# Optimization experiments

Hardware: AMD Instinct MI355X
Metric: run time of the kernel (lower is better)

The kernel has to match this reference:

```python
import jax, jax.numpy as jnp
import numpy as np
import math

B, T, Z, H, DOF = 256, 200, 64, 256, 12
NUM_LINKS = 13
POS_DIM = (NUM_LINKS + 1) * 3  # 42
TIME_BANDS = 6
TIME_DIM = 2 * TIME_BANDS + 1  # 13
ACTION_SCALE = 0.25
TRACK_ALPHA = 1.0
SIGMA_MIN, SIGMA_MAX = 0.05, 0.5


def setup_inputs() -> dict:
    key = jax.random.key(0)
    ks = iter(jax.random.split(key, 32))
    rn = lambda shape, s=0.1: jax.random.normal(next(ks), shape, jnp.float32) * s
    inp = {
        'z': jax.random.normal(next(ks), (B, Z), jnp.float32),
        'W_hz': rn((H, Z)), 'b_hz': rn((H,)),
        'W_cz': rn((H, Z)), 'b_cz': rn((H,)),
        'Wih': rn((4 * H, DOF + Z + TIME_DIM)), 'Whh': rn((4 * H, H)),
        'bih': rn((4 * H,)), 'bhh': rn((4 * H,)),
        'Wp1': rn((H, H)), 'bp1': rn((H,)),
        'Wp2': rn((DOF, H)), 'bp2': rn((DOF,)),
        'Wo1': rn((H, H)), 'bo1': rn((H,)),
        'Wo2': rn((3, H)), 'bo2': rn((3,)),
        'Wv': rn((POS_DIM, H)), 'bv': rn((POS_DIM,)),
        'Wfk': rn((NUM_LINKS * 3, DOF)), 'bfk': rn((NUM_LINKS * 3,)),
        'pos_mean': jax.random.normal(next(ks), (NUM_LINKS + 1, 3), jnp.float32),
        'pos_std': 0.5 + jax.random.uniform(next(ks), (NUM_LINKS + 1, 3), jnp.float32),
        'joint_lower': -jnp.ones((DOF,), jnp.float32),
        'joint_upper': jnp.ones((DOF,), jnp.float32),
        'default_dof_pos': jnp.zeros((DOF,), jnp.float32),
    }
    return inp


def _time_features():
    t = jnp.linspace(0.0, 1.0, T)
    feats = [t]
    for k in range(TIME_BANDS):
        f = 2.0 ** k
        feats.append(jnp.sin(2 * math.pi * f * t))
        feats.append(jnp.cos(2 * math.pi * f * t))
    return jnp.stack(feats, axis=-1)  # [T, TIME_DIM]


def reference(z, W_hz, b_hz, W_cz, b_cz, Wih, Whh, bih, bhh,
              Wp1, bp1, Wp2, bp2, Wo1, bo1, Wo2, bo2, Wv, bv, Wfk, bfk,
              pos_mean, pos_std, joint_lower, joint_upper, default_dof_pos):
    joint_range = (joint_upper - joint_lower) / 2.0
    joint_mean = (joint_upper + joint_lower) / 2.0
    time_feats = _time_features()  # [T, TIME_DIM]

    h0 = z @ W_hz.T + b_hz  # [B,H]
    c0 = z @ W_cz.T + b_cz
    prev0 = jnp.broadcast_to(default_dof_pos, (B, DOF))

    def step(carry, tf):
        h, c, prev = carry
        prev_norm = (prev - joint_mean) / joint_range
        x = jnp.concatenate([prev_norm, z, jnp.broadcast_to(tf, (B, TIME_DIM))], axis=-1)
        g = x @ Wih.T + bih + h @ Whh.T + bhh  # [B,4H]
        i, f, gg, o = jnp.split(g, 4, axis=-1)
        c_new = jax.nn.sigmoid(f) * c + jax.nn.sigmoid(i) * jnp.tanh(gg)
        h_new = jax.nn.sigmoid(o) * jnp.tanh(c_new)
        action = jnp.tanh(jax.nn.relu(h_new @ Wp1.T + bp1) @ Wp2.T + bp2)
        target = action * ACTION_SCALE + default_dof_pos
        cur = prev + TRACK_ALPHA * (target - prev)
        clamped = jnp.clip(cur, joint_lower, joint_upper)
        cur_in = cur + jax.lax.stop_gradient(clamped - cur)  # straight-through clamp
        obj = jax.nn.relu(h_new @ Wo1.T + bo1) @ Wo2.T + bo2
        return (h_new, c_new, jax.lax.stop_gradient(cur_in)), (h_new, action, cur, obj)

    _, (H_seq, actions, joints, objs) = jax.lax.scan(step, (h0, c0, prev0), time_feats)
    # [T,B,*] -> [B,T,*]
    H_seq = jnp.swapaxes(H_seq, 0, 1)
    actions_seq = jnp.swapaxes(actions, 0, 1)
    joint_traj = jnp.swapaxes(joints, 0, 1)
    object_traj = jnp.swapaxes(objs, 0, 1)

    agent_traj = joint_traj @ Wfk.T + bfk  # FK: [B,T,39]
    combined = jnp.concatenate([agent_traj, object_traj], axis=-1)  # [B,T,42]
    combined_rs = combined.reshape(B, T, NUM_LINKS + 1, 3)
    graph_x_mu = ((combined_rs - pos_mean) / pos_std).reshape(B, T, POS_DIM)

    sigma = SIGMA_MIN + (SIGMA_MAX - SIGMA_MIN) * jax.nn.sigmoid(H_seq @ Wv.T + bv)
    log_sigma_pos = jnp.log(sigma)
    return (graph_x_mu, joint_traj, actions_seq, log_sigma_pos)
```

## Files before the change

kernel.cpp:

```cpp
#include <hip/hip_runtime.h>
#include <math.h>

#define B_ 256
#define T_ 200
#define H_ 256
#define DOF_ 12

typedef __bf16 bf16;
typedef __bf16 bf16x8 __attribute__((ext_vector_type(8)));
typedef float f32x4 __attribute__((ext_vector_type(4)));

#define XK 288
#define XPAD 296
#define P1PAD 264

#define PI_D 3.14159265358979323846

#define OFF_TF     0u
#define OFF_TCONP  10400u
#define OFF_ZCP    829600u
#define OFF_H0     1878176u
#define OFF_C0     2140320u
#define OFF_WCOMB  2402464u
#define OFF_WP1    2992288u
#define OFF_WP2    3123360u
#define OFF_WO1    3131552u
#define OFF_WO2    3262624u
#define OFF_WV     3270816u
#define OFF_HX     3295392u
#define OFF_FLAGS  3557536u
#define OFF_HSEQ   3558400u

__device__ __forceinline__ float sigf(float x) { return 1.f / (1.f + __expf(-x)); }
__device__ __forceinline__ float tanh_f(float x) {
  float a = fabsf(x);
  float e = __expf(-2.f * a);
  float t = (1.f - e) / (1.f + e);
  return x < 0.f ? -t : t;
}

#define LBAR() asm volatile("s_waitcnt lgkmcnt(0)\n\ts_barrier" ::: "memory")

__global__ void k_zflags(unsigned int* flags) {
  int i = threadIdx.x;
  if (i < 32)
    __hip_atomic_store(&flags[i], 0u, __ATOMIC_RELAXED, __HIP_MEMORY_SCOPE_AGENT);
}

__global__ void k_tfeat(float* tf) {
  int i = blockIdx.x * blockDim.x + threadIdx.x;
  if (i >= T_ * 13) return;
  int t = i / 13, j = i % 13;
  float tv = (float)t / 199.f;
  float v;
  if (j == 0) v = tv;
  else {
    int k = (j - 1) >> 1;
    float f = (float)(1 << k);
    double arg = 2.0 * PI_D * (double)f * (double)tv;
    v = (j & 1) ? (float)sin(arg) : (float)cos(arg);
  }
  tf[i] = v;
}

__global__ void k_prep(const float* __restrict__ tf, const float* __restrict__ Wih,
                       const float* __restrict__ z,
                       const float* __restrict__ bih, const float* __restrict__ bhh,
                       const float* __restrict__ Whz, const float* __restrict__ bhz,
                       const float* __restrict__ Wcz, const float* __restrict__ bcz,
                       float* tconp, float* zcp, float* h0, float* c0) {
  int i = blockIdx.x * blockDim.x + threadIdx.x;
  if (i < 204800) {
    int g = i & 3, q = i >> 2;
    int m = q & 127, hm = (q >> 7) & 1, t = q >> 8;
    int n = g * 256 + 128 * hm + m;
    float s = 0.f;
    #pragma unroll
    for (int j = 0; j < 13; ++j) s += tf[t * 13 + j] * Wih[n * 89 + 76 + j];
    tconp[i] = s;
    return;
  }
  i -= 204800;
  if (i < 262144) {
    int r = i & 3, g = (i >> 2) & 3, tid = (i >> 4) & 511;
    int half = (i >> 13) & 1, pairk = i >> 14;
    int wv = tid >> 6, lr = tid & 15, lq = (tid >> 4) & 3;
    int b = pairk * 16 + lq * 4 + r;
    int n = g * 256 + 128 * half + 16 * wv + lr;
    float s = bih[n] + bhh[n];
    for (int k = 0; k < 64; ++k) s += z[b * 64 + k] * Wih[n * 89 + 12 + k];
    zcp[i] = s;
    return;
  }
  i -= 262144;
  if (i < 65536) {
    int b = i / 256, u = i % 256;
    float s = bhz[u];
    for (int k = 0; k < 64; ++k) s += z[b * 64 + k] * Whz[u * 64 + k];
    h0[i] = s;
    return;
  }
  i -= 65536;
  if (i < 65536) {
    int b = i / 256, u = i % 256;
    float s = bcz[u];
    for (int k = 0; k < 64; ++k) s += z[b * 64 + k] * Wcz[u * 64 + k];
    c0[i] = s;
  }
}

__global__ void k_cast(const float* __restrict__ Whh, const float* __restrict__ Wih,
                       const float* __restrict__ Wp1, const float* __restrict__ Wp2,
                       const float* __restrict__ Wo1, const float* __restrict__ Wo2,
                       const float* __restrict__ Wv,
                       bf16* Wcomb, bf16* Wp1b, bf16* Wp2b, bf16* Wo1b,
                       bf16* Wo2b, bf16* Wvb) {
  int i = blockIdx.x * blockDim.x + threadIdx.x;
  if (i < 294912) {
    int n = i / XK, k = i % XK;
    float v = (k < 256) ? Whh[n * 256 + k]
            : ((k < 268) ? Wih[n * 89 + (k - 256)] : 0.f);
    Wcomb[i] = (bf16)v;
    return;
  }
  i -= 294912;
  if (i < 65536) { Wp1b[i] = (bf16)Wp1[i]; return; }
  i -= 65536;
  if (i < 4096) { int r = i / 256; Wp2b[i] = (bf16)((r < 12) ? Wp2[i] : 0.f); return; }
  i -= 4096;
  if (i < 65536) { Wo1b[i] = (bf16)Wo1[i]; return; }
  i -= 65536;
  if (i < 4096) { int r = i / 256; Wo2b[i] = (bf16)((r < 3) ? Wo2[i] : 0.f); return; }
  i -= 4096;
  if (i < 12288) { int r = i / 256; Wvb[i] = (bf16)((r < 42) ? Wv[i] : 0.f); }
}

__global__ __launch_bounds__(512, 2) void k_recur(
    const float* __restrict__ zcp, const float* __restrict__ tconp,
    const float* __restrict__ h0, const float* __restrict__ c0,
    const bf16* __restrict__ Wcomb, const bf16* __restrict__ Wp1b,
    const bf16* __restrict__ Wp2b,
    const float* __restrict__ bp1, const float* __restrict__ bp2,
    const float* __restrict__ jlo, const float* __restrict__ jhi,
    const float* __restrict__ ddp,
    unsigned long long* hx, unsigned int* flags,
    bf16* __restrict__ Hseq, float* __restrict__ outJ, float* __restrict__ outA) {
  __shared__ bf16 xbuf[16][XPAD];
  __shared__ bf16 w1[272][P1PAD];
  __shared__ bf16 p1buf[16][P1PAD];
  const int tid = threadIdx.x;
  const int wv = tid >> 6, ln = tid & 63, lr = ln & 15, lq = ln >> 4;
  const int bid = blockIdx.x, pairk = bid >> 1, half = bid & 1;
  const int b0 = pairk * 16;
  const int u_loc = 16 * wv + lr;
  const int u_gl = 128 * half + u_loc;

  for (int i = tid; i < 272 * 32; i += 512) {
    int r = i >> 5, c8 = (i & 31) * 8;
    bf16x8 v = (r < 256)
      ? *reinterpret_cast<const bf16x8*>(&Wp1b[r * 256 + c8])
      : *reinterpret_cast<const bf16x8*>(&Wp2b[(r - 256) * 256 + c8]);
    *reinterpret_cast<bf16x8*>(&w1[r][c8]) = v;
  }
  for (int i = tid; i < 16 * XPAD; i += 512) {
    int r = i / XPAD, c = i % XPAD;
    float v = 0.f;
    if (c < 256) v = h0[(b0 + r) * 256 + c];
    else if (c < 268) {
      int d = c - 256;
      float lo = jlo[d], hi = jhi[d];
      v = (ddp[d] - 0.5f * (hi + lo)) / (0.5f * (hi - lo));
    }
    xbuf[r][c] = (bf16)v;
  }

  bf16x8 wc[4][9];
  #pragma unroll
  for (int g = 0; g < 4; ++g)
    #pragma unroll
    for (int kt = 0; kt < 9; ++kt) {
      wc[g][kt] = *reinterpret_cast<const bf16x8*>(
          &Wcomb[(size_t)(g * 256 + u_gl) * XK + kt * 32 + lq * 8]);
      f32x4 tmp = __builtin_bit_cast(f32x4, wc[g][kt]);
      asm volatile("" : "+v"(tmp));
      wc[g][kt] = __builtin_bit_cast(bf16x8, tmp);
    }

  float c_reg[4];
  #pragma unroll
  for (int r = 0; r < 4; ++r) c_reg[r] = c0[(b0 + lq * 4 + r) * 256 + u_gl];
  f32x4 zcreg[4];
  #pragma unroll
  for (int g = 0; g < 4; ++g)
    zcreg[g] = *reinterpret_cast<const f32x4*>(
        zcp + ((size_t)bid * 512 + tid) * 16 + g * 4);
  const float* tcb = tconp + (size_t)(half * 512 + u_loc * 4);
  const float bp1r0 = bp1[32 * wv + lr];
  const float bp1r1 = bp1[32 * wv + 16 + lr];
  float bp2r = 0.f, ddr = 0.f, lor = -1.f, hir = 1.f;
  if (lr < 12) { bp2r = bp2[lr]; ddr = ddp[lr]; lor = jlo[lr]; hir = jhi[lr]; }
  const float jmr = 0.5f * (hir + lor), jrr = 0.5f * (hir - lor);
  bf16* hs = Hseq + ((size_t)(b0 + lq * 4) * T_) * 256 + u_gl;

  unsigned int* pf = &flags[bid ^ 1];
  unsigned int* myf = &flags[bid];
  const int ru = tid >> 2, rc = tid & 3;
  const int rcol = 128 * (half ^ 1) + ru;

  f32x4 tcv = *reinterpret_cast<const f32x4*>(tcb);
  __syncthreads();
  bool dead = false;

  for (int t = 0; t < T_; ++t) {
    bf16x8 a[9];
    #pragma unroll
    for (int kt = 0; kt < 9; ++kt)
      a[kt] = *reinterpret_cast<const bf16x8*>(&xbuf[lr][kt * 32 + lq * 8]);
    LBAR();

    f32x4 ac[4];
    #pragma unroll
    for (int g = 0; g < 4; ++g) {
      ac[g] = zcreg[g] + tcv[g];
      #pragma unroll
      for (int kt = 0; kt < 9; ++kt)
        ac[g] = __builtin_amdgcn_mfma_f32_16x16x32_bf16(a[kt], wc[g][kt], ac[g], 0, 0, 0);
    }

    union { unsigned long long v; unsigned short s[4]; } pk;
    bf16 hb4[4];
    #pragma unroll
    for (int r = 0; r < 4; ++r) {
      float cn = sigf(ac[1][r]) * c_reg[r] + sigf(ac[0][r]) * tanh_f(ac[2][r]);
      float hn = sigf(ac[3][r]) * tanh_f(cn);
      c_reg[r] = cn;
      bf16 hb = (bf16)hn;
      hb4[r] = hb;
      xbuf[lq * 4 + r][u_gl] = hb;
      pk.s[r] = __builtin_bit_cast(unsigned short, hb);
    }
    __hip_atomic_store(
        &hx[(((size_t)(pairk * 2 + (t & 1)) * 2 + half) * 128 + u_loc) * 4 + lq],
        pk.v, __ATOMIC_RELAXED, __HIP_MEMORY_SCOPE_AGENT);
    asm volatile("s_waitcnt vmcnt(0)" ::: "memory");
    __builtin_amdgcn_s_barrier();
    const unsigned int want = t + 1;
    if (tid == 0)
      __hip_atomic_store(myf, want, __ATOMIC_RELAXED, __HIP_MEMORY_SCOPE_AGENT);
    #pragma unroll
    for (int r = 0; r < 4; ++r)
      hs[(size_t)r * (T_ * 256) + (size_t)t * 256] = hb4[r];
    f32x4 tcn = *reinterpret_cast<const f32x4*>(
        tcb + (size_t)((t + 1 < T_) ? t + 1 : t) * 1024);

    if (!dead) {
      int guard = 1 << 20;
      for (;;) {
        unsigned int fv =
            __hip_atomic_load(pf, __ATOMIC_RELAXED, __HIP_MEMORY_SCOPE_AGENT);
        if ((int)(fv - want) >= 0) break;
        if (--guard == 0) { dead = true; break; }
      }
    }
    unsigned long long pv = __hip_atomic_load(
        &hx[(((size_t)(pairk * 2 + (t & 1)) * 2 + (half ^ 1)) * 128 + ru) * 4 + rc],
        __ATOMIC_RELAXED, __HIP_MEMORY_SCOPE_AGENT);
    {
      unsigned short* ph = (unsigned short*)&pv;
      #pragma unroll
      for (int j = 0; j < 4; ++j)
        xbuf[rc * 4 + j][rcol] = __builtin_bit_cast(bf16, ph[j]);
    }
    LBAR();

    #pragma unroll
    for (int jn = 0; jn < 2; ++jn) {
      int n0 = 32 * wv + 16 * jn;
      float bb = (jn == 0) ? bp1r0 : bp1r1;
      f32x4 acc = {bb, bb, bb, bb};
      #pragma unroll
      for (int kt = 0; kt < 8; ++kt) {
        bf16x8 av = *reinterpret_cast<const bf16x8*>(&xbuf[lr][kt * 32 + lq * 8]);
        bf16x8 bv = *reinterpret_cast<const bf16x8*>(&w1[n0 + lr][kt * 32 + lq * 8]);
        acc = __builtin_amdgcn_mfma_f32_16x16x32_bf16(av, bv, acc, 0, 0, 0);
      }
      #pragma unroll
      for (int r = 0; r < 4; ++r)
        p1buf[lq * 4 + r][n0 + lr] = (bf16)fmaxf(acc[r], 0.f);
    }
    LBAR();

    if (wv == 0) {
      f32x4 acc = {0.f, 0.f, 0.f, 0.f};
      #pragma unroll
      for (int kt = 0; kt < 8; ++kt) {
        bf16x8 ap = *reinterpret_cast<const bf16x8*>(&p1buf[lr][kt * 32 + lq * 8]);
        bf16x8 w2 = *reinterpret_cast<const bf16x8*>(&w1[256 + lr][kt * 32 + lq * 8]);
        acc = __builtin_amdgcn_mfma_f32_16x16x32_bf16(ap, w2, acc, 0, 0, 0);
      }
      if (lr < 12) {
        #pragma unroll
        for (int r = 0; r < 4; ++r) {
          int b = lq * 4 + r;
          float act = tanh_f(acc[r] + bp2r);
          float curp = act * 0.25f + ddr;
          float cl = fminf(fmaxf(curp, lor), hir);
          if (half == 0) {
            size_t o = ((size_t)(b0 + b) * T_ + t) * 12 + lr;
            outA[o] = act;
            outJ[o] = curp;
          }
          xbuf[b][256 + lr] = (bf16)((cl - jmr) / jrr);
        }
      }
    }
    LBAR();
    tcv = tcn;
  }
}

__global__ __launch_bounds__(256) void k_post(
    const bf16* __restrict__ Hseq, const bf16* __restrict__ Wo1b,
    const bf16* __restrict__ Wo2b, const bf16* __restrict__ Wvb,
    const float* __restrict__ bo1, const float* __restrict__ bo2,
    const float* __restrict__ bv,
    const float* __restrict__ Wfk, const float* __restrict__ bfk,
    const float* __restrict__ pm, const float* __restrict__ ps,
    const float* __restrict__ joints, float* __restrict__ out0,
    float* __restrict__ out3) {
  __shared__ bf16 u1buf[16][P1PAD];
  __shared__ float objbuf[16][3];
  __shared__ float jbuf[16][12];
  const int tid = threadIdx.x;
  const int wv = tid >> 6;
  const int ln = tid & 63;
  const int lr = ln & 15;
  const int lq = ln >> 4;

  bf16x8 wo1f[4][8];
  float bo1r[4];
  #pragma unroll
  for (int jn = 0; jn < 4; ++jn) {
    int n0 = wv * 64 + jn * 16;
    bo1r[jn] = bo1[n0 + lr];
    #pragma unroll
    for (int kt = 0; kt < 8; ++kt)
      wo1f[jn][kt] = *reinterpret_cast<const bf16x8*>(
          &Wo1b[(size_t)(n0 + lr) * 256 + kt * 32 + lq * 8]);
  }
  const int col = (wv - 1) * 16 + lr;
  bf16x8 wvf[8];
  float bvr = 0.f;
  if (wv >= 1) {
    #pragma unroll
    for (int kt = 0; kt < 8; ++kt)
      wvf[kt] = *reinterpret_cast<const bf16x8*>(
          &Wvb[(size_t)col * 256 + kt * 32 + lq * 8]);
    bvr = (col < 42) ? bv[col] : 0.f;
  }
  bf16x8 wo2f[8];
  if (wv == 0) {
    #pragma unroll
    for (int kt = 0; kt < 8; ++kt)
      wo2f[kt] = *reinterpret_cast<const bf16x8*>(
          &Wo2b[(size_t)lr * 256 + kt * 32 + lq * 8]);
  }

  for (int it = 0; it < 10; ++it) {
    int tt = blockIdx.x * 10 + it;
    size_t r0 = (size_t)tt * 16;
    bf16x8 ah[8];
    #pragma unroll
    for (int kt = 0; kt < 8; ++kt)
      ah[kt] = *reinterpret_cast<const bf16x8*>(&Hseq[(r0 + lr) * 256 + kt * 32 + lq * 8]);
    #pragma unroll
    for (int jn = 0; jn < 4; ++jn) {
      int n0 = wv * 64 + jn * 16;
      float bb = bo1r[jn];
      f32x4 acc = {bb, bb, bb, bb};
      #pragma unroll
      for (int kt = 0; kt < 8; ++kt)
        acc = __builtin_amdgcn_mfma_f32_16x16x32_bf16(ah[kt], wo1f[jn][kt], acc, 0, 0, 0);
      #pragma unroll
      for (int r = 0; r < 4; ++r)
        u1buf[lq * 4 + r][n0 + lr] = (bf16)fmaxf(acc[r], 0.f);
    }
    if (wv >= 1) {
      f32x4 acc = {bvr, bvr, bvr, bvr};
      #pragma unroll
      for (int kt = 0; kt < 8; ++kt)
        acc = __builtin_amdgcn_mfma_f32_16x16x32_bf16(ah[kt], wvf[kt], acc, 0, 0, 0);
      if (col < 42) {
        #pragma unroll
        for (int r = 0; r < 4; ++r) {
          float s = 0.05f + 0.45f * sigf(acc[r]);
          out3[(r0 + lq * 4 + r) * 42 + col] = __logf(s);
        }
      }
    }
    if (tid < 192) {
      int rr = tid / 12, d = tid % 12;
      jbuf[rr][d] = joints[(r0 + rr) * 12 + d];
    }
    __syncthreads();
    if (wv == 0) {
      bf16x8 ap[8];
      #pragma unroll
      for (int kt = 0; kt < 8; ++kt)
        ap[kt] = *reinterpret_cast<const bf16x8*>(&u1buf[lr][kt * 32 + lq * 8]);
      f32x4 acc = {0.f, 0.f, 0.f, 0.f};
      #pragma unroll
      for (int kt = 0; kt < 8; ++kt)
        acc = __builtin_amdgcn_mfma_f32_16x16x32_bf16(ap[kt], wo2f[kt], acc, 0, 0, 0);
      if (lr < 3) {
        #pragma unroll
        for (int r = 0; r < 4; ++r)
          objbuf[lq * 4 + r][lr] = acc[r] + bo2[lr];
      }
    }
    __syncthreads();
    for (int e = tid; e < 16 * 42; e += 256) {
      int rr = e / 42, pd = e % 42;
      float v;
      if (pd < 39) {
        float s = bfk[pd];
        #pragma unroll
        for (int d = 0; d < 12; ++d) s += jbuf[rr][d] * Wfk[pd * 12 + d];
        v = s;
      } else v = objbuf[rr][pd - 39];
      out0[(r0 + rr) * 42 + pd] = (v - pm[pd]) / ps[pd];
    }
    __syncthreads();
  }
}

extern "C" void kernel_launch(void* const* d_in, const int* in_sizes, int n_in,
                              void* d_out, int out_size, void* d_ws, size_t ws_size,
                              hipStream_t stream) {
  const float* z   = (const float*)d_in[0];
  const float* Whz = (const float*)d_in[1];
  const float* bhz = (const float*)d_in[2];
  const float* Wcz = (const float*)d_in[3];
  const float* bcz = (const float*)d_in[4];
  const float* Wih = (const float*)d_in[5];
  const float* Whh = (const float*)d_in[6];
  const float* bih = (const float*)d_in[7];
  const float* bhh = (const float*)d_in[8];
  const float* Wp1 = (const float*)d_in[9];
  const float* bp1 = (const float*)d_in[10];
  const float* Wp2 = (const float*)d_in[11];
  const float* bp2 = (const float*)d_in[12];
  const float* Wo1 = (const float*)d_in[13];
  const float* bo1 = (const float*)d_in[14];
  const float* Wo2 = (const float*)d_in[15];
  const float* bo2 = (const float*)d_in[16];
  const float* Wv  = (const float*)d_in[17];
  const float* bv  = (const float*)d_in[18];
  const float* Wfk = (const float*)d_in[19];
  const float* bfk = (const float*)d_in[20];
  const float* pm  = (const float*)d_in[21];
  const float* ps  = (const float*)d_in[22];
  const float* jlo = (const float*)d_in[23];
  const float* jhi = (const float*)d_in[24];
  const float* ddp = (const float*)d_in[25];

  char* ws = (char*)d_ws;
  float* tf    = (float*)(ws + OFF_TF);
  float* tconp = (float*)(ws + OFF_TCONP);
  float* zcp   = (float*)(ws + OFF_ZCP);
  float* h0    = (float*)(ws + OFF_H0);
  float* c0    = (float*)(ws + OFF_C0);
  bf16* Wcomb  = (bf16*)(ws + OFF_WCOMB);
  bf16* Wp1b   = (bf16*)(ws + OFF_WP1);
  bf16* Wp2b   = (bf16*)(ws + OFF_WP2);
  bf16* Wo1b   = (bf16*)(ws + OFF_WO1);
  bf16* Wo2b   = (bf16*)(ws + OFF_WO2);
  bf16* Wvb    = (bf16*)(ws + OFF_WV);
  unsigned long long* hx = (unsigned long long*)(ws + OFF_HX);
  unsigned int* flags    = (unsigned int*)(ws + OFF_FLAGS);
  bf16* Hseq   = (bf16*)(ws + OFF_HSEQ);

  float* out  = (float*)d_out;
  float* out0 = out;
  float* outJ = out + 2150400;
  float* outA = out + 2764800;
  float* out3 = out + 3379200;

  k_zflags<<<1, 64, 0, stream>>>(flags);
  k_tfeat<<<11, 256, 0, stream>>>(tf);
  k_prep<<<2336, 256, 0, stream>>>(tf, Wih, z, bih, bhh, Whz, bhz, Wcz, bcz,
                                   tconp, zcp, h0, c0);
  k_cast<<<1744, 256, 0, stream>>>(Whh, Wih, Wp1, Wp2, Wo1, Wo2, Wv,
                                   Wcomb, Wp1b, Wp2b, Wo1b, Wo2b, Wvb);
  k_recur<<<32, 512, 0, stream>>>(zcp, tconp, h0, c0, Wcomb, Wp1b, Wp2b,
                                  bp1, bp2, jlo, jhi, ddp, hx, flags,
                                  Hseq, outJ, outA);
  k_post<<<320, 256, 0, stream>>>(Hseq, Wo1b, Wo2b, Wvb, bo1, bo2, bv,
                                  Wfk, bfk, pm, ps, outJ, out0, out3);
}
```

Before: 1.205 ms.

## Use per-wave flags for cross-block handoff and interleave MFMA chains

The block-wide barrier before publishing the flag is dropped. Each wave now sets and polls its own flag and reads only the partner rows its own wave consumes, so waves sync independently with the partner block. Partner blocks are remapped to bid^8, likely to place them on particular XCDs or CUs. The gate and p1 MFMA loops are reordered so four or two independent accumulators interleave, which hides MFMA latency. This adds more flags and polling traffic, and the spin guard is shortened.

```diff
diff --git a/kernel.cpp b/kernel.cpp
--- a/kernel.cpp
+++ b/kernel.cpp
@@ -27,8 +27,8 @@
 #define OFF_WO1    3131552u
 #define OFF_WO2    3262624u
 #define OFF_WV     3270816u
+#define OFF_FLAGS  (OFF_WV + 21504u)
 #define OFF_HX     3295392u
-#define OFF_FLAGS  3557536u
 #define OFF_HSEQ   3558400u
 
 __device__ __forceinline__ float sigf(float x) { return 1.f / (1.f + __expf(-x)); }
@@ -43,7 +43,7 @@
 
 __global__ void k_zflags(unsigned int* flags) {
   int i = threadIdx.x;
-  if (i < 32)
+  if (i < 256)
     __hip_atomic_store(&flags[i], 0u, __ATOMIC_RELAXED, __HIP_MEMORY_SCOPE_AGENT);
 }
 
@@ -135,7 +135,8 @@
   if (i < 12288) { int r = i / 256; Wvb[i] = (bf16)((r < 42) ? Wv[i] : 0.f); }
 }
 
-__global__ __launch_bounds__(512, 2) void k_recur(
+__global__ __launch_bounds__(512)
+__attribute__((amdgpu_waves_per_eu(2, 2))) void k_recur(
     const float* __restrict__ zcp, const float* __restrict__ tconp,
     const float* __restrict__ h0, const float* __restrict__ c0,
     const bf16* __restrict__ Wcomb, const bf16* __restrict__ Wp1b,
@@ -150,7 +151,11 @@
   __shared__ bf16 p1buf[16][P1PAD];
   const int tid = threadIdx.x;
   const int wv = tid >> 6, ln = tid & 63, lr = ln & 15, lq = ln >> 4;
-  const int bid = blockIdx.x, pairk = bid >> 1, half = bid & 1;
+  const int bid = blockIdx.x;
+  const int pairk = ((bid >> 4) << 3) | (bid & 7);
+  const int half = (bid >> 3) & 1;
+  const int lbid = pairk * 2 + half;
+  const int pbid = bid ^ 8;
   const int b0 = pairk * 16;
   const int u_loc = 16 * wv + lr;
   const int u_gl = 128 * half + u_loc;
@@ -193,7 +198,7 @@
   #pragma unroll
   for (int g = 0; g < 4; ++g)
     zcreg[g] = *reinterpret_cast<const f32x4*>(
-        zcp + ((size_t)bid * 512 + tid) * 16 + g * 4);
+        zcp + ((size_t)lbid * 512 + tid) * 16 + g * 4);
   const float* tcb = tconp + (size_t)(half * 512 + u_loc * 4);
   const float bp1r0 = bp1[32 * wv + lr];
   const float bp1r1 = bp1[32 * wv + 16 + lr];
@@ -202,30 +207,31 @@
   const float jmr = 0.5f * (hir + lor), jrr = 0.5f * (hir - lor);
   bf16* hs = Hseq + ((size_t)(b0 + lq * 4) * T_) * 256 + u_gl;
 
-  unsigned int* pf = &flags[bid ^ 1];
-  unsigned int* myf = &flags[bid];
-  const int ru = tid >> 2, rc = tid & 3;
-  const int rcol = 128 * (half ^ 1) + ru;
+  unsigned int* myf = &flags[bid * 8 + wv];
+  unsigned int* pf  = &flags[pbid * 8 + wv];
+  const int wru = 16 * wv + (ln >> 2), wrc = ln & 3;
+  const int rcol = 128 * (half ^ 1) + wru;
+  unsigned long long* hxw0 = &hx[(((size_t)(pairk * 2 + 0) * 2 + half) * 128 + u_loc) * 4 + lq];
+  unsigned long long* hxw1 = &hx[(((size_t)(pairk * 2 + 1) * 2 + half) * 128 + u_loc) * 4 + lq];
+  unsigned long long* hxr0 = &hx[(((size_t)(pairk * 2 + 0) * 2 + (half ^ 1)) * 128 + wru) * 4 + wrc];
+  unsigned long long* hxr1 = &hx[(((size_t)(pairk * 2 + 1) * 2 + (half ^ 1)) * 128 + wru) * 4 + wrc];
 
   f32x4 tcv = *reinterpret_cast<const f32x4*>(tcb);
   __syncthreads();
   bool dead = false;
 
   for (int t = 0; t < T_; ++t) {
-    bf16x8 a[9];
-    #pragma unroll
-    for (int kt = 0; kt < 9; ++kt)
-      a[kt] = *reinterpret_cast<const bf16x8*>(&xbuf[lr][kt * 32 + lq * 8]);
+    f32x4 ac[4];
+    #pragma unroll
+    for (int g = 0; g < 4; ++g) ac[g] = zcreg[g] + tcv[g];
+    #pragma unroll
+    for (int kt = 0; kt < 9; ++kt) {
+      bf16x8 a = *reinterpret_cast<const bf16x8*>(&xbuf[lr][kt * 32 + lq * 8]);
+      #pragma unroll
+      for (int g = 0; g < 4; ++g)
+        ac[g] = __builtin_amdgcn_mfma_f32_16x16x32_bf16(a, wc[g][kt], ac[g], 0, 0, 0);
+    }
     LBAR();
-
-    f32x4 ac[4];
-    #pragma unroll
-    for (int g = 0; g < 4; ++g) {
-      ac[g] = zcreg[g] + tcv[g];
-      #pragma unroll
-      for (int kt = 0; kt < 9; ++kt)
-        ac[g] = __builtin_amdgcn_mfma_f32_16x16x32_bf16(a[kt], wc[g][kt], ac[g], 0, 0, 0);
-    }
 
     union { unsigned long long v; unsigned short s[4]; } pk;
     bf16 hb4[4];
@@ -239,13 +245,11 @@
       xbuf[lq * 4 + r][u_gl] = hb;
       pk.s[r] = __builtin_bit_cast(unsigned short, hb);
     }
-    __hip_atomic_store(
-        &hx[(((size_t)(pairk * 2 + (t & 1)) * 2 + half) * 128 + u_loc) * 4 + lq],
-        pk.v, __ATOMIC_RELAXED, __HIP_MEMORY_SCOPE_AGENT);
+    __hip_atomic_store((t & 1) ? hxw1 : hxw0, pk.v,
+                       __ATOMIC_RELAXED, __HIP_MEMORY_SCOPE_AGENT);
     asm volatile("s_waitcnt vmcnt(0)" ::: "memory");
-    __builtin_amdgcn_s_barrier();
     const unsigned int want = t + 1;
-    if (tid == 0)
+    if (ln == 0)
       __hip_atomic_store(myf, want, __ATOMIC_RELAXED, __HIP_MEMORY_SCOPE_AGENT);
     #pragma unroll
     for (int r = 0; r < 4; ++r)
@@ -254,7 +258,7 @@
         tcb + (size_t)((t + 1 < T_) ? t + 1 : t) * 1024);
 
     if (!dead) {
-      int guard = 1 << 20;
+      int guard = 1 << 18;
       for (;;) {
         unsigned int fv =
             __hip_atomic_load(pf, __ATOMIC_RELAXED, __HIP_MEMORY_SCOPE_AGENT);
@@ -262,31 +266,33 @@
         if (--guard == 0) { dead = true; break; }
       }
     }
-    unsigned long long pv = __hip_atomic_load(
-        &hx[(((size_t)(pairk * 2 + (t & 1)) * 2 + (half ^ 1)) * 128 + ru) * 4 + rc],
-        __ATOMIC_RELAXED, __HIP_MEMORY_SCOPE_AGENT);
+    unsigned long long pv = __hip_atomic_load((t & 1) ? hxr1 : hxr0,
+                                              __ATOMIC_RELAXED,
+                                              __HIP_MEMORY_SCOPE_AGENT);
     {
       unsigned short* ph = (unsigned short*)&pv;
       #pragma unroll
       for (int j = 0; j < 4; ++j)
-        xbuf[rc * 4 + j][rcol] = __builtin_bit_cast(bf16, ph[j]);
+        xbuf[wrc * 4 + j][rcol] = __builtin_bit_cast(bf16, ph[j]);
     }
     LBAR();
 
-    #pragma unroll
-    for (int jn = 0; jn < 2; ++jn) {
-      int n0 = 32 * wv + 16 * jn;
-      float bb = (jn == 0) ? bp1r0 : bp1r1;
-      f32x4 acc = {bb, bb, bb, bb};
+    {
+      f32x4 acc0 = {bp1r0, bp1r0, bp1r0, bp1r0};
+      f32x4 acc1 = {bp1r1, bp1r1, bp1r1, bp1r1};
       #pragma unroll
       for (int kt = 0; kt < 8; ++kt) {
         bf16x8 av = *reinterpret_cast<const bf16x8*>(&xbuf[lr][kt * 32 + lq * 8]);
-        bf16x8 bv = *reinterpret_cast<const bf16x8*>(&w1[n0 + lr][kt * 32 + lq * 8]);
-        acc = __builtin_amdgcn_mfma_f32_16x16x32_bf16(av, bv, acc, 0, 0, 0);
-      }
-      #pragma unroll
-      for (int r = 0; r < 4; ++r)
-        p1buf[lq * 4 + r][n0 + lr] = (bf16)fmaxf(acc[r], 0.f);
+        bf16x8 b0v = *reinterpret_cast<const bf16x8*>(&w1[32 * wv + lr][kt * 32 + lq * 8]);
+        bf16x8 b1v = *reinterpret_cast<const bf16x8*>(&w1[32 * wv + 16 + lr][kt * 32 + lq * 8]);
+        acc0 = __builtin_amdgcn_mfma_f32_16x16x32_bf16(av, b0v, acc0, 0, 0, 0);
+        acc1 = __builtin_amdgcn_mfma_f32_16x16x32_bf16(av, b1v, acc1, 0, 0, 0);
+      }
+      #pragma unroll
+      for (int r = 0; r < 4; ++r) {
+        p1buf[lq * 4 + r][32 * wv + lr] = (bf16)fmaxf(acc0[r], 0.f);
+        p1buf[lq * 4 + r][32 * wv + 16 + lr] = (bf16)fmaxf(acc1[r], 0.f);
+      }
     }
     LBAR();
 
@@ -486,7 +492,7 @@
   float* outA = out + 2764800;
   float* out3 = out + 3379200;
 
-  k_zflags<<<1, 64, 0, stream>>>(flags);
+  k_zflags<<<1, 256, 0, stream>>>(flags);
   k_tfeat<<<11, 256, 0, stream>>>(tf);
   k_prep<<<2336, 256, 0, stream>>>(tf, Wih, z, bih, bhh, Whz, bhz, Wcz, bcz,
                                    tconp, zcp, h0, c0);
```

Measured after the change: 1.122 ms. -6.9%, faster.
